# Kernel tuning notes

Measured on AMD Instinct MI355X. Metric: run time of the kernel, lower is better.

Reference implementation:

```python
import jax, jax.numpy as jnp
import numpy as np

H, D = 16, 64  # num_heads, head_dim (hidden=1024)


def _rel_shift(x):
    # Transformer-XL skewing: x [B,H,T,L] -> shifted [B,H,T,T]
    B, Hh, T, L = x.shape
    x = jnp.pad(x, ((0, 0), (0, 0), (0, 0), (1, 0)))
    x = x.reshape(B, Hh, L + 1, T)[:, :, 1:, :]
    return x.reshape(B, Hh, T, L)[:, :, :, :T]


def setup_inputs() -> dict:
    key = jax.random.key(0)
    ks = jax.random.split(key, 9)
    B, T, hid = 2, 2048, 1024
    s = 0.02
    return {
        "x": jax.random.normal(ks[0], (B, T, hid), jnp.float32),
        "pos_emb": jax.random.normal(ks[1], (T, hid), jnp.float32),
        "Wq": jax.random.normal(ks[2], (hid, hid), jnp.float32) * s,
        "Wk": jax.random.normal(ks[3], (hid, hid), jnp.float32) * s,
        "Wv": jax.random.normal(ks[4], (hid, hid), jnp.float32) * s,
        "Wo": jax.random.normal(ks[5], (hid, hid), jnp.float32) * s,
        "Wrel": jax.random.normal(ks[6], (hid, hid), jnp.float32) * s,
        "bias_u": jax.random.normal(ks[7], (H, D), jnp.float32) * s,
        "bias_v": jax.random.normal(ks[8], (H, D), jnp.float32) * s,
    }


def reference(x, pos_emb, Wq, Wk, Wv, Wo, Wrel, bias_u, bias_v):
    B, T, hid = x.shape
    scale = D ** (-0.5)
    # projections (torch Linear: y = x @ W.T), reshape to [B,H,T,D]
    q = (x @ Wq.T).reshape(B, T, H, D).transpose(0, 2, 1, 3)
    k = (x @ Wk.T).reshape(B, T, H, D).transpose(0, 2, 1, 3)
    v = (x @ Wv.T).reshape(B, T, H, D).transpose(0, 2, 1, 3)
    # content score with bias_u
    content = jnp.einsum('bhtd,bhsd->bhts', q + bias_u[None, :, None, :], k)
    # positional score with bias_v against projected relative keys [H,L,D]
    rel_k = (pos_emb @ Wrel.T).reshape(-1, H, D).transpose(1, 0, 2)
    pos_score = jnp.einsum('bhtd,hld->bhtl', q + bias_v[None, :, None, :], rel_k)
    pos_score = _rel_shift(pos_score)
    scores = (content + pos_score) * scale
    attn = jax.nn.softmax(scores, axis=-1)
    out = jnp.einsum('bhts,bhsd->bhtd', attn, v)
    out = out.transpose(0, 2, 1, 3).reshape(B, T, hid)
    return out @ Wo.T
```

## Files before the change

### kernel.cpp

```cpp
#include <hip/hip_runtime.h>
#include <hip/hip_bf16.h>

#define T_SEQ 2048
#define HID   1024
#define NH    16
#define HD    64
#define NB    2

typedef __bf16 bf16_t;
typedef bf16_t bf16x8 __attribute__((ext_vector_type(8)));
typedef bf16_t bf16x4 __attribute__((ext_vector_type(4)));
typedef float  f32x4  __attribute__((ext_vector_type(4)));

static __device__ __forceinline__ f32x4 mfma16(bf16x8 a, bf16x8 b, f32x4 c) {
    return __builtin_amdgcn_mfma_f32_16x16x32_bf16(a, b, c, 0, 0, 0);
}

static __device__ __forceinline__ void gll16(const bf16_t* g, bf16_t* l) {
    __builtin_amdgcn_global_load_lds(
        (const __attribute__((address_space(1))) void*)g,
        (__attribute__((address_space(3))) void*)l, 16, 0, 0);
}

__global__ __launch_bounds__(256) void cvt_all(
    const float* __restrict__ x, const float* __restrict__ pos,
    const float* __restrict__ wq, const float* __restrict__ wk,
    const float* __restrict__ wv, const float* __restrict__ wo,
    const float* __restrict__ wrel,
    bf16_t* __restrict__ xb, bf16_t* __restrict__ pb,
    bf16_t* __restrict__ wqb, bf16_t* __restrict__ wkb,
    bf16_t* __restrict__ wvb, bf16_t* __restrict__ wob,
    bf16_t* __restrict__ wrelb)
{
    int blk = blockIdx.x;
    const float* in; bf16_t* out;
    if (blk < 2048)      { in = x;   out = xb; }
    else if (blk < 3072) { in = pos; out = pb; blk -= 2048; }
    else {
        const int wi = (blk - 3072) >> 9; blk = (blk - 3072) & 511;
        switch (wi) {
            case 0:  in = wq;   out = wqb;   break;
            case 1:  in = wk;   out = wkb;   break;
            case 2:  in = wv;   out = wvb;   break;
            case 3:  in = wo;   out = wob;   break;
            default: in = wrel; out = wrelb; break;
        }
    }
    const int i = blk * 256 + threadIdx.x;
    const float4* p = (const float4*)(in + (size_t)i * 8);
    float4 a0 = p[0], a1 = p[1];
    bf16x8 v;
    v[0]=(bf16_t)a0.x; v[1]=(bf16_t)a0.y; v[2]=(bf16_t)a0.z; v[3]=(bf16_t)a0.w;
    v[4]=(bf16_t)a1.x; v[5]=(bf16_t)a1.y; v[6]=(bf16_t)a1.z; v[7]=(bf16_t)a1.w;
    *(bf16x8*)(out + (size_t)i * 8) = v;
}

template<int OMODE>
__global__ __launch_bounds__(256) void gemm_bb(const bf16_t* __restrict__ A,
                                               const bf16_t* __restrict__ W,
                                               void* __restrict__ outv, int M, int cpx) {
    const int hw = blockIdx.x;
    const int logical = (hw & 7) * cpx + (hw >> 3);
    const int mt = logical >> 3, nt = logical & 7;
    const int row0 = mt * 128, col0 = nt * 128;
    const int tid = threadIdx.x;
    const int w = tid >> 6, lane = tid & 63;
    const int wr = (w >> 1) * 64, wc = (w & 1) * 64;
    const int lr = lane & 15, lkg = lane >> 4;
    const int kd = lkg * 8;

    __shared__ bf16_t Al[128*64];
    __shared__ bf16_t Bl[128*64];

    const int rsh   = lane >> 3;
    const int colSw = ((lane & 7) * 8) ^ (rsh << 3);
    const int rBase = 8*w + rsh;

    f32x4 acc[4][4] = {};

    for (int t = 0; t < 16; ++t) {
        const int k0 = t * 64;
        if (t) __syncthreads();
#pragma unroll
        for (int i = 0; i < 4; ++i) {
            const int r = rBase + 32*i;
            gll16(A + (size_t)(row0 + r)*HID + k0 + colSw, &Al[i*2048 + w*512]);
            gll16(W + (size_t)(col0 + r)*HID + k0 + colSw, &Bl[i*2048 + w*512]);
        }
        __syncthreads();
#pragma unroll
        for (int ks = 0; ks < 2; ++ks) {
            bf16x8 af[4], bq[4];
#pragma unroll
            for (int i = 0; i < 4; ++i) {
                const int ar = wr + i*16 + lr;
                af[i] = *(const bf16x8*)&Al[ar*64 + ((ks*32 + kd) ^ ((ar & 7) << 3))];
                const int br = wc + i*16 + lr;
                bq[i] = *(const bf16x8*)&Bl[br*64 + ((ks*32 + kd) ^ ((br & 7) << 3))];
            }
#pragma unroll
            for (int i = 0; i < 4; ++i)
#pragma unroll
                for (int j = 0; j < 4; ++j)
                    acc[i][j] = mfma16(af[i], bq[j], acc[i][j]);
        }
    }

    const int rb = lkg * 4;
#pragma unroll
    for (int i = 0; i < 4; ++i) {
#pragma unroll
        for (int j = 0; j < 4; ++j) {
            const int col = col0 + wc + j*16 + lr;
            const int row = row0 + wr + i*16 + rb;
            if (OMODE == 0) {
                bf16_t* ob = (bf16_t*)outv;
#pragma unroll
                for (int r = 0; r < 4; ++r)
                    ob[(size_t)(row + r) * HID + col] = (bf16_t)acc[i][j][r];
            } else if (OMODE == 1) {
                const int bb = row >> 11, tt = row & (T_SEQ - 1);
                const int hh = col >> 6,  d = col & 63;
                bf16x4 pk;
#pragma unroll
                for (int r = 0; r < 4; ++r) pk[r] = (bf16_t)acc[i][j][r];
                *(bf16x4*)((bf16_t*)outv + ((size_t)((bb*NH + hh)*HD + d))*T_SEQ + tt) = pk;
            } else {
                float* of = (float*)outv;
#pragma unroll
                for (int r = 0; r < 4; ++r)
                    of[(size_t)(row + r) * HID + col] = acc[i][j][r];
            }
        }
    }
}

template<int NSPLIT>
__global__ __launch_bounds__(256) void attn_kernel(
    const bf16_t* __restrict__ Q, const bf16_t* __restrict__ K,
    const bf16_t* __restrict__ VT, const bf16_t* __restrict__ RK,
    const float* __restrict__ bias_u, const float* __restrict__ bias_v,
    bf16_t* __restrict__ AO, float* __restrict__ PO, float* __restrict__ ML,
    int cpx)
{
    const int hw = blockIdx.x;
    const int logical = (hw & 7) * cpx + (hw >> 3);
    const int tile = logical & 31;
    int h, b, split;
    if (NSPLIT == 1) {
        split = 0; h = (logical >> 5) & 15; b = logical >> 9;
    } else {
        split = (logical >> 5) & 1; h = (logical >> 6) & 15; b = logical >> 10;
    }

    const int w = threadIdx.x >> 6, lane = threadIdx.x & 63;
    const int t0 = tile * 64;
    const int lr = lane & 15, lkg = lane >> 4;
    const int kd = lkg * 8;

    __shared__ bf16_t Kl[64*64];
    __shared__ bf16_t Vl[64*64];
    __shared__ bf16_t R1l[128*64];
    __shared__ bf16_t R2l[128*64];
    __shared__ float  pp[4][16][84];
    __shared__ bf16_t pl[4][16][72];

    const int tb = t0 + w * 16;

    bf16x8 aqu[2], aqv[2], aqv2[2];
    {
        const int t  = tb + lr;
        const int t2 = (t + 1 < T_SEQ) ? t + 1 : T_SEQ - 1;
        const bf16_t* qp  = Q + ((size_t)(b*T_SEQ + t )*NH + h)*HD;
        const bf16_t* qp2 = Q + ((size_t)(b*T_SEQ + t2)*NH + h)*HD;
        const float* bu = bias_u + h*HD;
        const float* bv = bias_v + h*HD;
#pragma unroll
        for (int f = 0; f < 2; ++f) {
            const int k0 = f*32 + kd;
            bf16x8 q1 = *(const bf16x8*)(qp  + k0);
            bf16x8 q2 = *(const bf16x8*)(qp2 + k0);
#pragma unroll
            for (int j = 0; j < 8; ++j) {
                const float fu = bu[k0+j], fv = bv[k0+j];
                aqu [f][j] = (bf16_t)(((float)q1[j] + fu) * 0.125f);
                aqv [f][j] = (bf16_t)(((float)q1[j] + fv) * 0.125f);
                aqv2[f][j] = (bf16_t)(((float)q2[j] + fv) * 0.125f);
            }
        }
    }

    float m_run = -1e30f, l_run = 0.0f;
    f32x4 oacc[4];
    f32x4 zf = {0.f, 0.f, 0.f, 0.f};
#pragma unroll
    for (int nf = 0; nf < 4; ++nf) oacc[nf] = zf;

    const bf16_t* Kb = K  + (size_t)(b*T_SEQ)*HID + h*HD;
    const bf16_t* Vb = VT + (size_t)((b*NH + h)*HD)*T_SEQ;
    const bf16_t* Rb = RK + h*HD;
    const int d15 = 15 - lr;
    const int sBeg = split * (T_SEQ / NSPLIT);

    const int rsh   = lane >> 3;
    const int colSw = ((lane & 7) * 8) ^ (rsh << 3);
    const int kvRow = 16*w + rsh;
    const int rRow  = 32*w + rsh;

    for (int ss = 0; ss < T_SEQ / NSPLIT; ss += 64) {
        const int s0 = sBeg + ss;
        const int r1base = s0 - t0 + T_SEQ - 64;
        const int r2base = s0 - t0 - 65;
        const bool anyB1 = (s0 <= t0 + 63);
        const bool anyB2 = (s0 >= t0 - 61);

        __syncthreads();
#pragma unroll
        for (int i = 0; i < 2; ++i) {
            const int r = kvRow + 8*i;
            gll16(Kb + (size_t)(s0 + r)*HID + colSw, &Kl[(2*w + i)*512]);
            gll16(Vb + (size_t)r*T_SEQ + s0 + colSw, &Vl[(2*w + i)*512]);
        }
        if (anyB1) {
#pragma unroll
            for (int i = 0; i < 4; ++i) {
                const long g = (long)(r1base + rRow + 8*i);
                gll16(Rb + g*HID + colSw, &R1l[(4*w + i)*512]);
            }
        }
        if (anyB2) {
#pragma unroll
            for (int i = 0; i < 4; ++i) {
                const long g = (long)(r2base + rRow + 8*i);
                gll16(Rb + g*HID + colSw, &R2l[(4*w + i)*512]);
            }
        }
        __syncthreads();

        f32x4 sc[4];
#pragma unroll
        for (int j = 0; j < 4; ++j) {
            const int row = j*16 + lr;
            const int sw = (row & 7) << 3;
            bf16x8 a0 = *(const bf16x8*)&Kl[row*64 + (kd ^ sw)];
            bf16x8 a1 = *(const bf16x8*)&Kl[row*64 + ((32 + kd) ^ sw)];
            sc[j] = mfma16(a1, aqu[1], mfma16(a0, aqu[0], zf));
        }

        if (s0 <= tb + 15) {
#pragma unroll
            for (int jf = 0; jf < 5; ++jf) {
                const int rr = 48 - 16*w + jf*16 + lr;
                const int sw = (rr & 7) << 3;
                bf16x8 a0 = *(const bf16x8*)&R1l[rr*64 + (kd ^ sw)];
                bf16x8 a1 = *(const bf16x8*)&R1l[rr*64 + ((32 + kd) ^ sw)];
                f32x4 c = mfma16(a1, aqv[1], mfma16(a0, aqv[0], zf));
                *(f32x4*)&pp[w][lr][jf*16 + 4*lkg] = c;
            }
            if (s0 <= tb - 63) {
#pragma unroll
                for (int j = 0; j < 4; ++j)
#pragma unroll
                    for (int r = 0; r < 4; ++r)
                        sc[j][r] += pp[w][lr][16*j + 4*lkg + r + d15];
            } else {
#pragma unroll
                for (int j = 0; j < 4; ++j)
#pragma unroll
                    for (int r = 0; r < 4; ++r) {
                        const int sof = 16*j + 4*lkg + r;
                        const int dt  = (s0 + sof) - (tb + lr);
                        const float v = pp[w][lr][sof + d15];
                        sc[j][r] += (dt <= 0) ? v : 0.0f;
                    }
            }
        }
        if (s0 >= tb - 61) {
#pragma unroll
            for (int jf = 0; jf < 5; ++jf) {
                const int rr = 48 - 16*w + jf*16 + lr;
                const int sw = (rr & 7) << 3;
                bf16x8 a0 = *(const bf16x8*)&R2l[rr*64 + (kd ^ sw)];
                bf16x8 a1 = *(const bf16x8*)&R2l[rr*64 + ((32 + kd) ^ sw)];
                f32x4 c = mfma16(a1, aqv2[1], mfma16(a0, aqv2[0], zf));
                *(f32x4*)&pp[w][lr][jf*16 + 4*lkg] = c;
            }
            if (s0 >= tb + 17) {
#pragma unroll
                for (int j = 0; j < 4; ++j)
#pragma unroll
                    for (int r = 0; r < 4; ++r)
                        sc[j][r] += pp[w][lr][16*j + 4*lkg + r + d15];
            } else {
#pragma unroll
                for (int j = 0; j < 4; ++j)
#pragma unroll
                    for (int r = 0; r < 4; ++r) {
                        const int sof = 16*j + 4*lkg + r;
                        const int dt  = (s0 + sof) - (tb + lr);
                        const float v = pp[w][lr][sof + d15];
                        sc[j][r] += (dt >= 2) ? v : 0.0f;
                    }
            }
        }

        float mx = fmaxf(fmaxf(fmaxf(sc[0][0], sc[0][1]), fmaxf(sc[0][2], sc[0][3])),
                         fmaxf(fmaxf(sc[1][0], sc[1][1]), fmaxf(sc[1][2], sc[1][3])));
        mx = fmaxf(mx, fmaxf(fmaxf(fmaxf(sc[2][0], sc[2][1]), fmaxf(sc[2][2], sc[2][3])),
                             fmaxf(fmaxf(sc[3][0], sc[3][1]), fmaxf(sc[3][2], sc[3][3]))));
        mx = fmaxf(mx, __shfl_xor(mx, 16, 64));
        mx = fmaxf(mx, __shfl_xor(mx, 32, 64));
        const float mnew = fmaxf(m_run, mx);
        const float fac = __expf(m_run - mnew);
        float sum = 0.0f;
#pragma unroll
        for (int j = 0; j < 4; ++j) {
            bf16x4 pk;
#pragma unroll
            for (int r = 0; r < 4; ++r) {
                const float p = __expf(sc[j][r] - mnew);
                sum += p;
                pk[r] = (bf16_t)p;
            }
            *(bf16x4*)&pl[w][lr][16*j + 4*lkg] = pk;
        }
        sum += __shfl_xor(sum, 16, 64);
        sum += __shfl_xor(sum, 32, 64);
        l_run = l_run * fac + sum;
        m_run = mnew;

#pragma unroll
        for (int r = 0; r < 4; ++r) {
            const float facq = __shfl(fac, 4*lkg + r, 64);
#pragma unroll
            for (int nf = 0; nf < 4; ++nf) oacc[nf][r] *= facq;
        }

        bf16x8 pa0 = *(const bf16x8*)(&pl[w][lr][kd]);
        bf16x8 pa1 = *(const bf16x8*)(&pl[w][lr][32 + kd]);
#pragma unroll
        for (int nf = 0; nf < 4; ++nf) {
            const int row = nf*16 + lr;
            const int sw = (row & 7) << 3;
            bf16x8 b0 = *(const bf16x8*)&Vl[row*64 + (kd ^ sw)];
            bf16x8 b1 = *(const bf16x8*)&Vl[row*64 + ((32 + kd) ^ sw)];
            oacc[nf] = mfma16(pa1, b1, mfma16(pa0, b0, oacc[nf]));
        }
    }

    if (NSPLIT == 1) {
        const float linv = 1.0f / l_run;
#pragma unroll
        for (int r = 0; r < 4; ++r) {
            const float lq = __shfl(linv, 4*lkg + r, 64);
            const int t = tb + 4*lkg + r;
#pragma unroll
            for (int nf = 0; nf < 4; ++nf)
                AO[(size_t)(b*T_SEQ + t)*HID + h*HD + nf*16 + lr] = (bf16_t)(oacc[nf][r] * lq);
        }
    } else {
        float* po = PO + (((size_t)split*NB*NH + b*NH + h)*T_SEQ)*HD;
#pragma unroll
        for (int r = 0; r < 4; ++r)
#pragma unroll
            for (int nf = 0; nf < 4; ++nf)
                po[(size_t)(tb + 4*lkg + r)*HD + nf*16 + lr] = oacc[nf][r];
        if (lkg == 0) {
            float* ml = ML + ((size_t)split*NB*NH + b*NH + h)*2*T_SEQ;
            ml[tb + lr] = m_run;
            ml[T_SEQ + tb + lr] = l_run;
        }
    }
}

__global__ __launch_bounds__(256) void combine_kernel(
    const float* __restrict__ PO, const float* __restrict__ ML,
    bf16_t* __restrict__ AO)
{
    const int idx = blockIdx.x * 256 + threadIdx.x;
    const int t = idx & (T_SEQ - 1);
    const int h = (idx >> 11) & (NH - 1);
    const int b = idx >> 15;
    const size_t poS = (size_t)NB*NH*T_SEQ*HD;
    const size_t mlS = (size_t)NB*NH*2*T_SEQ;
    const float* po1 = PO + (((size_t)b*NH + h)*T_SEQ + t)*HD;
    const float* po2 = po1 + poS;
    const float* ml1 = ML + ((size_t)b*NH + h)*2*T_SEQ;
    const float* ml2 = ml1 + mlS;
    const float m1 = ml1[t], l1 = ml1[T_SEQ + t];
    const float m2 = ml2[t], l2 = ml2[T_SEQ + t];
    const float M  = fmaxf(m1, m2);
    float f1 = __expf(m1 - M), f2 = __expf(m2 - M);
    const float linv = 1.0f / (f1*l1 + f2*l2);
    f1 *= linv; f2 *= linv;
    bf16_t* ao = AO + ((size_t)b*T_SEQ + t)*HID + h*HD;
#pragma unroll
    for (int d = 0; d < HD; d += 8) {
        f32x4 a0 = *(const f32x4*)(po1 + d), a1 = *(const f32x4*)(po1 + d + 4);
        f32x4 c0 = *(const f32x4*)(po2 + d), c1 = *(const f32x4*)(po2 + d + 4);
        bf16x8 o;
#pragma unroll
        for (int j = 0; j < 4; ++j) {
            o[j]     = (bf16_t)(f1*a0[j] + f2*c0[j]);
            o[4 + j] = (bf16_t)(f1*a1[j] + f2*c1[j]);
        }
        *(bf16x8*)(ao + d) = o;
    }
}

extern "C" void kernel_launch(void* const* d_in, const int* in_sizes, int n_in,
                              void* d_out, int out_size, void* d_ws, size_t ws_size,
                              hipStream_t stream) {
    const float* x    = (const float*)d_in[0];
    const float* pos  = (const float*)d_in[1];
    const float* Wq   = (const float*)d_in[2];
    const float* Wk   = (const float*)d_in[3];
    const float* Wv   = (const float*)d_in[4];
    const float* Wo   = (const float*)d_in[5];
    const float* Wrel = (const float*)d_in[6];
    const float* bu   = (const float*)d_in[7];
    const float* bv   = (const float*)d_in[8];

    bf16_t* ws   = (bf16_t*)d_ws;
    const size_t M1 = 1024u * 1024u;
    bf16_t* qb    = ws;
    bf16_t* kb    = ws + 4*M1;
    bf16_t* vtb   = ws + 8*M1;
    bf16_t* rkb   = ws + 12*M1;
    bf16_t* ab    = ws + 14*M1;
    bf16_t* xb    = ab;
    bf16_t* pb    = ws + 18*M1;
    bf16_t* wqb   = ws + 20*M1;
    bf16_t* wkb   = ws + 21*M1;
    bf16_t* wvb   = ws + 22*M1;
    bf16_t* wob   = ws + 23*M1;
    bf16_t* wrelb = ws + 24*M1;

    const size_t baseBytes = 25*M1*2;
    const size_t poBytes = (size_t)2*NB*NH*T_SEQ*HD*4;
    const size_t mlBytes = (size_t)2*NB*NH*2*T_SEQ*4;
    float* PO = (float*)((char*)d_ws + baseBytes);
    float* ML = (float*)((char*)d_ws + baseBytes + poBytes);
    const bool split2 = ws_size >= baseBytes + poBytes + mlBytes;

    cvt_all<<<5632, 256, 0, stream>>>(x, pos, Wq, Wk, Wv, Wo, Wrel,
                                      xb, pb, wqb, wkb, wvb, wob, wrelb);

    gemm_bb<0><<<256, 256, 0, stream>>>(xb, wqb,   qb,  4096, 32);
    gemm_bb<0><<<256, 256, 0, stream>>>(xb, wkb,   kb,  4096, 32);
    gemm_bb<1><<<256, 256, 0, stream>>>(xb, wvb,   vtb, 4096, 32);
    gemm_bb<0><<<128, 256, 0, stream>>>(pb, wrelb, rkb, 2048, 16);

    if (split2) {
        attn_kernel<2><<<2048, 256, 0, stream>>>(qb, kb, vtb, rkb, bu, bv, ab, PO, ML, 256);
        combine_kernel<<<256, 256, 0, stream>>>(PO, ML, ab);
    } else {
        attn_kernel<1><<<1024, 256, 0, stream>>>(qb, kb, vtb, rkb, bu, bv, ab, nullptr, nullptr, 128);
    }

    gemm_bb<2><<<256, 256, 0, stream>>>(ab, wob, d_out, 4096, 32);
}
```

Measured before the change: 264.8 us.

## Fuse projection GEMMs, double-buffer GEMM LDS, drop attention split and shrink LDS

The four projection GEMMs are merged into one 896-block launch. The GEMM core now double-buffers its LDS tiles so the next K-tile load overlaps the current MFMA work. The attention kernel drops the 2-way sequence split and the combine kernel, uses a single relative-key LDS buffer that is reloaded when both bands are needed, and stores the positional partial scores in bf16 instead of fp32. Together these cut launch count and LDS footprint, which may raise occupancy. In exchange, parallelism in attention is halved, an extra sync/reload sits on diagonal tiles, and bf16 rounding of the positional scores costs some precision.

```diff
diff --git a/kernel.cpp b/kernel.cpp
--- a/kernel.cpp
+++ b/kernel.cpp
@@ -55,48 +55,51 @@
     *(bf16x8*)(out + (size_t)i * 8) = v;
 }
 
-template<int OMODE>
-__global__ __launch_bounds__(256) void gemm_bb(const bf16_t* __restrict__ A,
-                                               const bf16_t* __restrict__ W,
-                                               void* __restrict__ outv, int M, int cpx) {
-    const int hw = blockIdx.x;
-    const int logical = (hw & 7) * cpx + (hw >> 3);
-    const int mt = logical >> 3, nt = logical & 7;
-    const int row0 = mt * 128, col0 = nt * 128;
+static __device__ __forceinline__ void gemm_core(
+    bf16_t* Al, bf16_t* Bl,
+    const bf16_t* __restrict__ A, const bf16_t* __restrict__ W,
+    void* __restrict__ outv, int row0, int col0, int omode)
+{
     const int tid = threadIdx.x;
     const int w = tid >> 6, lane = tid & 63;
     const int wr = (w >> 1) * 64, wc = (w & 1) * 64;
     const int lr = lane & 15, lkg = lane >> 4;
     const int kd = lkg * 8;
-
-    __shared__ bf16_t Al[128*64];
-    __shared__ bf16_t Bl[128*64];
-
     const int rsh   = lane >> 3;
     const int colSw = ((lane & 7) * 8) ^ (rsh << 3);
     const int rBase = 8*w + rsh;
 
     f32x4 acc[4][4] = {};
 
+#pragma unroll
+    for (int i = 0; i < 4; ++i) {
+        const int r = rBase + 32*i;
+        gll16(A + (size_t)(row0 + r)*HID + colSw, &Al[i*2048 + w*512]);
+        gll16(W + (size_t)(col0 + r)*HID + colSw, &Bl[i*2048 + w*512]);
+    }
+    __syncthreads();
+
     for (int t = 0; t < 16; ++t) {
-        const int k0 = t * 64;
-        if (t) __syncthreads();
-#pragma unroll
-        for (int i = 0; i < 4; ++i) {
-            const int r = rBase + 32*i;
-            gll16(A + (size_t)(row0 + r)*HID + k0 + colSw, &Al[i*2048 + w*512]);
-            gll16(W + (size_t)(col0 + r)*HID + k0 + colSw, &Bl[i*2048 + w*512]);
-        }
-        __syncthreads();
+        const int cur = (t & 1) * 8192;
+        const int nxt = 8192 - cur;
+        if (t < 15) {
+            const int k0 = (t + 1) * 64;
+#pragma unroll
+            for (int i = 0; i < 4; ++i) {
+                const int r = rBase + 32*i;
+                gll16(A + (size_t)(row0 + r)*HID + k0 + colSw, &Al[nxt + i*2048 + w*512]);
+                gll16(W + (size_t)(col0 + r)*HID + k0 + colSw, &Bl[nxt + i*2048 + w*512]);
+            }
+        }
 #pragma unroll
         for (int ks = 0; ks < 2; ++ks) {
             bf16x8 af[4], bq[4];
 #pragma unroll
             for (int i = 0; i < 4; ++i) {
                 const int ar = wr + i*16 + lr;
-                af[i] = *(const bf16x8*)&Al[ar*64 + ((ks*32 + kd) ^ ((ar & 7) << 3))];
+                af[i] = *(const bf16x8*)&Al[cur + ar*64 + ((ks*32 + kd) ^ ((ar & 7) << 3))];
                 const int br = wc + i*16 + lr;
-                bq[i] = *(const bf16x8*)&Bl[br*64 + ((ks*32 + kd) ^ ((br & 7) << 3))];
+                bq[i] = *(const bf16x8*)&Bl[cur + br*64 + ((ks*32 + kd) ^ ((br & 7) << 3))];
             }
 #pragma unroll
             for (int i = 0; i < 4; ++i)
@@ -104,6 +107,7 @@
                 for (int j = 0; j < 4; ++j)
                     acc[i][j] = mfma16(af[i], bq[j], acc[i][j]);
         }
+        __syncthreads();
     }
 
     const int rb = lkg * 4;
@@ -113,12 +117,12 @@
         for (int j = 0; j < 4; ++j) {
             const int col = col0 + wc + j*16 + lr;
             const int row = row0 + wr + i*16 + rb;
-            if (OMODE == 0) {
+            if (omode == 0) {
                 bf16_t* ob = (bf16_t*)outv;
 #pragma unroll
                 for (int r = 0; r < 4; ++r)
                     ob[(size_t)(row + r) * HID + col] = (bf16_t)acc[i][j][r];
-            } else if (OMODE == 1) {
+            } else if (omode == 1) {
                 const int bb = row >> 11, tt = row & (T_SEQ - 1);
                 const int hh = col >> 6,  d = col & 63;
                 bf16x4 pk;
@@ -135,23 +139,49 @@
     }
 }
 
-template<int NSPLIT>
+__global__ __launch_bounds__(256) void gemm_proj(
+    const bf16_t* __restrict__ xb, const bf16_t* __restrict__ pb,
+    const bf16_t* __restrict__ wqb, const bf16_t* __restrict__ wkb,
+    const bf16_t* __restrict__ wvb, const bf16_t* __restrict__ wrelb,
+    bf16_t* __restrict__ qb, bf16_t* __restrict__ kb,
+    bf16_t* __restrict__ vtb, bf16_t* __restrict__ rkb)
+{
+    __shared__ bf16_t Al[2*128*64];
+    __shared__ bf16_t Bl[2*128*64];
+    const int hw = blockIdx.x;
+    const int logical = (hw & 7) * 112 + (hw >> 3);
+    const bf16_t* A; const bf16_t* W; void* out; int omode = 0; int l;
+    if (logical < 256)      { A = xb; W = wqb;   out = qb;  l = logical; }
+    else if (logical < 512) { A = xb; W = wkb;   out = kb;  l = logical - 256; }
+    else if (logical < 768) { A = xb; W = wvb;   out = vtb; l = logical - 512; omode = 1; }
+    else                    { A = pb; W = wrelb; out = rkb; l = logical - 768; }
+    const int row0 = (l >> 3) * 128, col0 = (l & 7) * 128;
+    gemm_core(Al, Bl, A, W, out, row0, col0, omode);
+}
+
+__global__ __launch_bounds__(256) void gemm_out(
+    const bf16_t* __restrict__ ab, const bf16_t* __restrict__ wob,
+    float* __restrict__ outp)
+{
+    __shared__ bf16_t Al[2*128*64];
+    __shared__ bf16_t Bl[2*128*64];
+    const int hw = blockIdx.x;
+    const int logical = (hw & 7) * 32 + (hw >> 3);
+    const int row0 = (logical >> 3) * 128, col0 = (logical & 7) * 128;
+    gemm_core(Al, Bl, ab, wob, outp, row0, col0, 2);
+}
+
 __global__ __launch_bounds__(256) void attn_kernel(
     const bf16_t* __restrict__ Q, const bf16_t* __restrict__ K,
     const bf16_t* __restrict__ VT, const bf16_t* __restrict__ RK,
     const float* __restrict__ bias_u, const float* __restrict__ bias_v,
-    bf16_t* __restrict__ AO, float* __restrict__ PO, float* __restrict__ ML,
-    int cpx)
+    bf16_t* __restrict__ AO)
 {
     const int hw = blockIdx.x;
-    const int logical = (hw & 7) * cpx + (hw >> 3);
+    const int logical = (hw & 7) * 128 + (hw >> 3);
     const int tile = logical & 31;
-    int h, b, split;
-    if (NSPLIT == 1) {
-        split = 0; h = (logical >> 5) & 15; b = logical >> 9;
-    } else {
-        split = (logical >> 5) & 1; h = (logical >> 6) & 15; b = logical >> 10;
-    }
+    const int h    = (logical >> 5) & 15;
+    const int b    = logical >> 9;
 
     const int w = threadIdx.x >> 6, lane = threadIdx.x & 63;
     const int t0 = tile * 64;
@@ -160,9 +190,8 @@
 
     __shared__ bf16_t Kl[64*64];
     __shared__ bf16_t Vl[64*64];
-    __shared__ bf16_t R1l[128*64];
-    __shared__ bf16_t R2l[128*64];
-    __shared__ float  pp[4][16][84];
+    __shared__ bf16_t Rl[128*64];
+    __shared__ bf16_t pp[4][16][84];
     __shared__ bf16_t pl[4][16][72];
 
     const int tb = t0 + w * 16;
@@ -200,15 +229,13 @@
     const bf16_t* Vb = VT + (size_t)((b*NH + h)*HD)*T_SEQ;
     const bf16_t* Rb = RK + h*HD;
     const int d15 = 15 - lr;
-    const int sBeg = split * (T_SEQ / NSPLIT);
 
     const int rsh   = lane >> 3;
     const int colSw = ((lane & 7) * 8) ^ (rsh << 3);
     const int kvRow = 16*w + rsh;
     const int rRow  = 32*w + rsh;
 
-    for (int ss = 0; ss < T_SEQ / NSPLIT; ss += 64) {
-        const int s0 = sBeg + ss;
+    for (int s0 = 0; s0 < T_SEQ; s0 += 64) {
         const int r1base = s0 - t0 + T_SEQ - 64;
         const int r2base = s0 - t0 - 65;
         const bool anyB1 = (s0 <= t0 + 63);
@@ -221,18 +248,12 @@
             gll16(Kb + (size_t)(s0 + r)*HID + colSw, &Kl[(2*w + i)*512]);
             gll16(Vb + (size_t)r*T_SEQ + s0 + colSw, &Vl[(2*w + i)*512]);
         }
-        if (anyB1) {
+        {
+            const int rb0 = anyB1 ? r1base : r2base;
 #pragma unroll
             for (int i = 0; i < 4; ++i) {
-                const long g = (long)(r1base + rRow + 8*i);
-                gll16(Rb + g*HID + colSw, &R1l[(4*w + i)*512]);
-            }
-        }
-        if (anyB2) {
-#pragma unroll
-            for (int i = 0; i < 4; ++i) {
-                const long g = (long)(r2base + rRow + 8*i);
-                gll16(Rb + g*HID + colSw, &R2l[(4*w + i)*512]);
+                const long g = (long)(rb0 + rRow + 8*i);
+                gll16(Rb + g*HID + colSw, &Rl[(4*w + i)*512]);
             }
         }
         __syncthreads();
@@ -252,17 +273,20 @@
             for (int jf = 0; jf < 5; ++jf) {
                 const int rr = 48 - 16*w + jf*16 + lr;
                 const int sw = (rr & 7) << 3;
-                bf16x8 a0 = *(const bf16x8*)&R1l[rr*64 + (kd ^ sw)];
-                bf16x8 a1 = *(const bf16x8*)&R1l[rr*64 + ((32 + kd) ^ sw)];
+                bf16x8 a0 = *(const bf16x8*)&Rl[rr*64 + (kd ^ sw)];
+                bf16x8 a1 = *(const bf16x8*)&Rl[rr*64 + ((32 + kd) ^ sw)];
                 f32x4 c = mfma16(a1, aqv[1], mfma16(a0, aqv[0], zf));
-                *(f32x4*)&pp[w][lr][jf*16 + 4*lkg] = c;
+                bf16x4 cb;
+#pragma unroll
+                for (int r = 0; r < 4; ++r) cb[r] = (bf16_t)c[r];
+                *(bf16x4*)&pp[w][lr][jf*16 + 4*lkg] = cb;
             }
             if (s0 <= tb - 63) {
 #pragma unroll
                 for (int j = 0; j < 4; ++j)
 #pragma unroll
                     for (int r = 0; r < 4; ++r)
-                        sc[j][r] += pp[w][lr][16*j + 4*lkg + r + d15];
+                        sc[j][r] += (float)pp[w][lr][16*j + 4*lkg + r + d15];
             } else {
 #pragma unroll
                 for (int j = 0; j < 4; ++j)
@@ -270,27 +294,41 @@
                     for (int r = 0; r < 4; ++r) {
                         const int sof = 16*j + 4*lkg + r;
                         const int dt  = (s0 + sof) - (tb + lr);
-                        const float v = pp[w][lr][sof + d15];
+                        const float v = (float)pp[w][lr][sof + d15];
                         sc[j][r] += (dt <= 0) ? v : 0.0f;
                     }
             }
         }
+
+        if (anyB1 && anyB2) {
+            __syncthreads();
+#pragma unroll
+            for (int i = 0; i < 4; ++i) {
+                const long g = (long)(r2base + rRow + 8*i);
+                gll16(Rb + g*HID + colSw, &Rl[(4*w + i)*512]);
+            }
+            __syncthreads();
+        }
+
         if (s0 >= tb - 61) {
 #pragma unroll
             for (int jf = 0; jf < 5; ++jf) {
                 const int rr = 48 - 16*w + jf*16 + lr;
                 const int sw = (rr & 7) << 3;
-                bf16x8 a0 = *(const bf16x8*)&R2l[rr*64 + (kd ^ sw)];
-                bf16x8 a1 = *(const bf16x8*)&R2l[rr*64 + ((32 + kd) ^ sw)];
+                bf16x8 a0 = *(const bf16x8*)&Rl[rr*64 + (kd ^ sw)];
+                bf16x8 a1 = *(const bf16x8*)&Rl[rr*64 + ((32 + kd) ^ sw)];
                 f32x4 c = mfma16(a1, aqv2[1], mfma16(a0, aqv2[0], zf));
-                *(f32x4*)&pp[w][lr][jf*16 + 4*lkg] = c;
+                bf16x4 cb;
+#pragma unroll
+                for (int r = 0; r < 4; ++r) cb[r] = (bf16_t)c[r];
+                *(bf16x4*)&pp[w][lr][jf*16 + 4*lkg] = cb;
             }
             if (s0 >= tb + 17) {
 #pragma unroll
                 for (int j = 0; j < 4; ++j)
 #pragma unroll
                     for (int r = 0; r < 4; ++r)
-                        sc[j][r] += pp[w][lr][16*j + 4*lkg + r + d15];
+                        sc[j][r] += (float)pp[w][lr][16*j + 4*lkg + r + d15];
             } else {
 #pragma unroll
                 for (int j = 0; j < 4; ++j)
@@ -298,7 +336,7 @@
                     for (int r = 0; r < 4; ++r) {
                         const int sof = 16*j + 4*lkg + r;
                         const int dt  = (s0 + sof) - (tb + lr);
-                        const float v = pp[w][lr][sof + d15];
+                        const float v = (float)pp[w][lr][sof + d15];
                         sc[j][r] += (dt >= 2) ? v : 0.0f;
                     }
             }
@@ -348,63 +386,14 @@
         }
     }
 
-    if (NSPLIT == 1) {
-        const float linv = 1.0f / l_run;
-#pragma unroll
-        for (int r = 0; r < 4; ++r) {
-            const float lq = __shfl(linv, 4*lkg + r, 64);
-            const int t = tb + 4*lkg + r;
-#pragma unroll
-            for (int nf = 0; nf < 4; ++nf)
-                AO[(size_t)(b*T_SEQ + t)*HID + h*HD + nf*16 + lr] = (bf16_t)(oacc[nf][r] * lq);
-        }
-    } else {
-        float* po = PO + (((size_t)split*NB*NH + b*NH + h)*T_SEQ)*HD;
-#pragma unroll
-        for (int r = 0; r < 4; ++r)
-#pragma unroll
-            for (int nf = 0; nf < 4; ++nf)
-                po[(size_t)(tb + 4*lkg + r)*HD + nf*16 + lr] = oacc[nf][r];
-        if (lkg == 0) {
-            float* ml = ML + ((size_t)split*NB*NH + b*NH + h)*2*T_SEQ;
-            ml[tb + lr] = m_run;
-            ml[T_SEQ + tb + lr] = l_run;
-        }
-    }
-}
-
-__global__ __launch_bounds__(256) void combine_kernel(
-    const float* __restrict__ PO, const float* __restrict__ ML,
-    bf16_t* __restrict__ AO)
-{
-    const int idx = blockIdx.x * 256 + threadIdx.x;
-    const int t = idx & (T_SEQ - 1);
-    const int h = (idx >> 11) & (NH - 1);
-    const int b = idx >> 15;
-    const size_t poS = (size_t)NB*NH*T_SEQ*HD;
-    const size_t mlS = (size_t)NB*NH*2*T_SEQ;
-    const float* po1 = PO + (((size_t)b*NH + h)*T_SEQ + t)*HD;
-    const float* po2 = po1 + poS;
-    const float* ml1 = ML + ((size_t)b*NH + h)*2*T_SEQ;
-    const float* ml2 = ml1 + mlS;
-    const float m1 = ml1[t], l1 = ml1[T_SEQ + t];
-    const float m2 = ml2[t], l2 = ml2[T_SEQ + t];
-    const float M  = fmaxf(m1, m2);
-    float f1 = __expf(m1 - M), f2 = __expf(m2 - M);
-    const float linv = 1.0f / (f1*l1 + f2*l2);
-    f1 *= linv; f2 *= linv;
-    bf16_t* ao = AO + ((size_t)b*T_SEQ + t)*HID + h*HD;
-#pragma unroll
-    for (int d = 0; d < HD; d += 8) {
-        f32x4 a0 = *(const f32x4*)(po1 + d), a1 = *(const f32x4*)(po1 + d + 4);
-        f32x4 c0 = *(const f32x4*)(po2 + d), c1 = *(const f32x4*)(po2 + d + 4);
-        bf16x8 o;
-#pragma unroll
-        for (int j = 0; j < 4; ++j) {
-            o[j]     = (bf16_t)(f1*a0[j] + f2*c0[j]);
-            o[4 + j] = (bf16_t)(f1*a1[j] + f2*c1[j]);
-        }
-        *(bf16x8*)(ao + d) = o;
+    const float linv = 1.0f / l_run;
+#pragma unroll
+    for (int r = 0; r < 4; ++r) {
+        const float lq = __shfl(linv, 4*lkg + r, 64);
+        const int t = tb + 4*lkg + r;
+#pragma unroll
+        for (int nf = 0; nf < 4; ++nf)
+            AO[(size_t)(b*T_SEQ + t)*HID + h*HD + nf*16 + lr] = (bf16_t)(oacc[nf][r] * lq);
     }
 }
 
@@ -436,27 +425,13 @@
     bf16_t* wob   = ws + 23*M1;
     bf16_t* wrelb = ws + 24*M1;
 
-    const size_t baseBytes = 25*M1*2;
-    const size_t poBytes = (size_t)2*NB*NH*T_SEQ*HD*4;
-    const size_t mlBytes = (size_t)2*NB*NH*2*T_SEQ*4;
-    float* PO = (float*)((char*)d_ws + baseBytes);
-    float* ML = (float*)((char*)d_ws + baseBytes + poBytes);
-    const bool split2 = ws_size >= baseBytes + poBytes + mlBytes;
-
     cvt_all<<<5632, 256, 0, stream>>>(x, pos, Wq, Wk, Wv, Wo, Wrel,
                                       xb, pb, wqb, wkb, wvb, wob, wrelb);
 
-    gemm_bb<0><<<256, 256, 0, stream>>>(xb, wqb,   qb,  4096, 32);
-    gemm_bb<0><<<256, 256, 0, stream>>>(xb, wkb,   kb,  4096, 32);
-    gemm_bb<1><<<256, 256, 0, stream>>>(xb, wvb,   vtb, 4096, 32);
-    gemm_bb<0><<<128, 256, 0, stream>>>(pb, wrelb, rkb, 2048, 16);
-
-    if (split2) {
-        attn_kernel<2><<<2048, 256, 0, stream>>>(qb, kb, vtb, rkb, bu, bv, ab, PO, ML, 256);
-        combine_kernel<<<256, 256, 0, stream>>>(PO, ML, ab);
-    } else {
-        attn_kernel<1><<<1024, 256, 0, stream>>>(qb, kb, vtb, rkb, bu, bv, ab, nullptr, nullptr, 128);
-    }
-
-    gemm_bb<2><<<256, 256, 0, stream>>>(ab, wob, d_out, 4096, 32);
-}
+    gemm_proj<<<896, 256, 0, stream>>>(xb, pb, wqb, wkb, wvb, wrelb,
+                                       qb, kb, vtb, rkb);
+
+    attn_kernel<<<1024, 256, 0, stream>>>(qb, kb, vtb, rkb, bu, bv, ab);
+
+    gemm_out<<<256, 256, 0, stream>>>(ab, wob, (float*)d_out);
+}
```

After: 273.6 us. 3.3% more time.
